# Kernel optimization log

Measured on AMD Instinct MI355X. Metric: run time of the kernel, lower is better.

The kernel has to match this reference:

```python
import jax, jax.numpy as jnp
import numpy as np

B = 65536
N_WORKER, N_PROJECT, EMB = 1807, 2490, 10
STATE_DIM = 2 * EMB          # 20
HIDDEN = 2 * STATE_DIM       # 40
ACTION_DIM = EMB             # 10


def setup_inputs() -> dict:
    key = jax.random.key(0)
    ks = jax.random.split(key, 8)
    worker_ids = jax.random.randint(ks[0], (B,), 0, N_WORKER)
    project_ids = jax.random.randint(ks[1], (B,), 0, N_PROJECT)
    worker_emb = jax.random.normal(ks[2], (N_WORKER, EMB), dtype=jnp.float32)
    project_emb = jax.random.normal(ks[3], (N_PROJECT, EMB), dtype=jnp.float32)
    W1 = jax.random.normal(ks[4], (HIDDEN, STATE_DIM), dtype=jnp.float32) / np.sqrt(STATE_DIM)
    b1 = jnp.zeros((HIDDEN,), dtype=jnp.float32)
    W2 = jax.random.normal(ks[5], (ACTION_DIM, HIDDEN), dtype=jnp.float32) / np.sqrt(HIDDEN)
    b2 = jnp.zeros((ACTION_DIM,), dtype=jnp.float32)
    return {"worker_ids": worker_ids, "project_ids": project_ids,
            "worker_emb": worker_emb, "project_emb": project_emb,
            "W1": W1, "b1": b1, "W2": W2, "b2": b2}


def reference(worker_ids, project_ids, worker_emb, project_emb, W1, b1, W2, b2):
    we = worker_emb[worker_ids]              # [B, 10]
    pe = project_emb[project_ids]            # [B, 10]
    x = jnp.concatenate([we, pe], axis=-1)   # [B, 20]
    h = jax.nn.relu(x @ W1.T + b1)           # [B, 40]
    the_weights = (h @ W2.T + b2)[:, None, :]  # [B, 1, 10]
    # original loop rebuilds rows 1..2489 of the project table -> single slice
    table = project_emb[1:N_PROJECT]         # [2489, 10]
    p = jnp.einsum('bqd,nd->bqn', the_weights, table)  # [B, 1, 2489]
    argmax = jnp.argmax(p, axis=2)           # [B, 1]
    return argmax + 1
```

## Files before the change

kernel.cpp:

```cpp
#include <hip/hip_runtime.h>
#include <float.h>

using v2f = __attribute__((ext_vector_type(2))) float;
using v4f = __attribute__((ext_vector_type(4))) float;

#define EMB 10
#define STATE 20
#define HIDDEN 40
#define NPROJ 2490
#define WAVES 16
#define ITEMS 128

__global__ __launch_bounds__(256, 4) void mlp_kernel(
    const int* __restrict__ wid, const int* __restrict__ pid,
    const float* __restrict__ wemb, const float* __restrict__ pemb,
    const float* __restrict__ W1, const float* __restrict__ b1,
    const float* __restrict__ W2, const float* __restrict__ b2,
    float* __restrict__ ws)
{
    const int b = blockIdx.x * 256 + threadIdx.x;

    const int wi = wid[b];
    const int pi = pid[b];
    const float* __restrict__ wr = wemb + wi * EMB;
    const float* __restrict__ pr = pemb + pi * EMB;
    v2f x2[STATE / 2];
    #pragma unroll
    for (int k = 0; k < EMB / 2; ++k) x2[k] = *(const v2f*)(wr + 2 * k);
    #pragma unroll
    for (int k = 0; k < EMB / 2; ++k) x2[EMB / 2 + k] = *(const v2f*)(pr + 2 * k);

    float hb[HIDDEN];
    #pragma unroll 4
    for (int j = 0; j < HIDDEN; ++j) {
        const v2f* w1r = (const v2f*)(W1 + j * STATE);
        v2f a = w1r[0] * x2[0];
        #pragma unroll
        for (int k = 1; k < STATE / 2; ++k) a += w1r[k] * x2[k];
        hb[j] = fmaxf(a.x + a.y + b1[j], 0.0f);
    }
    v2f h2[HIDDEN / 2];
    #pragma unroll
    for (int k = 0; k < HIDDEN / 2; ++k) h2[k] = (v2f){hb[2 * k], hb[2 * k + 1]};

    v2f* wout = (v2f*)(ws + b * EMB);
    #pragma unroll
    for (int d = 0; d < EMB; d += 2) {
        const v2f* w2r0 = (const v2f*)(W2 + d * HIDDEN);
        const v2f* w2r1 = (const v2f*)(W2 + (d + 1) * HIDDEN);
        v2f a0 = w2r0[0] * h2[0];
        v2f a1 = w2r1[0] * h2[0];
        #pragma unroll
        for (int k = 1; k < HIDDEN / 2; ++k) { a0 += w2r0[k] * h2[k]; a1 += w2r1[k] * h2[k]; }
        wout[d / 2] = (v2f){a0.x + a0.y + b2[d], a1.x + a1.y + b2[d + 1]};
    }
}

__device__ __forceinline__ void score_row(const float* __restrict__ tr, int row,
                                          const float w0[10], const float w1[10],
                                          float best[2], int bidx[2]) {
    float t0 = tr[0], t1 = tr[1], t2 = tr[2], t3 = tr[3], t4 = tr[4];
    float t5 = tr[5], t6 = tr[6], t7 = tr[7], t8 = tr[8], t9 = tr[9];

    float e0 = t0 * w0[0];
    float o0 = t1 * w0[1];
    e0 = fmaf(t2, w0[2], e0);  o0 = fmaf(t3, w0[3], o0);
    e0 = fmaf(t4, w0[4], e0);  o0 = fmaf(t5, w0[5], o0);
    e0 = fmaf(t6, w0[6], e0);  o0 = fmaf(t7, w0[7], o0);
    e0 = fmaf(t8, w0[8], e0);  o0 = fmaf(t9, w0[9], o0);
    float s0 = e0 + o0;

    float e1 = t0 * w1[0];
    float o1 = t1 * w1[1];
    e1 = fmaf(t2, w1[2], e1);  o1 = fmaf(t3, w1[3], o1);
    e1 = fmaf(t4, w1[4], e1);  o1 = fmaf(t5, w1[5], o1);
    e1 = fmaf(t6, w1[6], e1);  o1 = fmaf(t7, w1[7], o1);
    e1 = fmaf(t8, w1[8], e1);  o1 = fmaf(t9, w1[9], o1);
    float s1 = e1 + o1;

    if (s0 > best[0]) { best[0] = s0; bidx[0] = row; }
    if (s1 > best[1]) { best[1] = s1; bidx[1] = row; }
}

template <int P0, int P1>
__device__ __forceinline__ void scan_range(const float* __restrict__ tblf,
                                           const float w0[10], const float w1[10],
                                           float best[2], int bidx[2]) {
    const float* t = tblf + P0 * 20;
    #pragma unroll 4
    for (int p = P0; p < P1; ++p, t += 20) {
        score_row(t,      2 * p,     w0, w1, best, bidx);
        score_row(t + 10, 2 * p + 1, w0, w1, best, bidx);
    }
}

__global__ __launch_bounds__(1024, 8) void scan_kernel(
    const float* __restrict__ pemb, const float* __restrict__ ws,
    int* __restrict__ out)
{
    __shared__ float sb[WAVES][ITEMS];
    __shared__ int   si[WAVES][ITEMS];

    const int tid  = threadIdx.x;
    const int lane = tid & 63;
    const int wave = tid >> 6;
    const int itemBase = blockIdx.x * ITEMS;

    const float* __restrict__ tblf = pemb;

    float w0[10], w1[10];
    {
        const v4f* s0 = (const v4f*)(ws + (itemBase + lane) * EMB);
        const v2f* s0t = (const v2f*)(ws + (itemBase + lane) * EMB + 8);
        v4f a = s0[0], b = s0[1]; v2f c = s0t[0];
        w0[0]=a.x; w0[1]=a.y; w0[2]=a.z; w0[3]=a.w;
        w0[4]=b.x; w0[5]=b.y; w0[6]=b.z; w0[7]=b.w;
        w0[8]=c.x; w0[9]=c.y;
        const v4f* s1 = (const v4f*)(ws + (itemBase + 64 + lane) * EMB);
        const v2f* s1t = (const v2f*)(ws + (itemBase + 64 + lane) * EMB + 8);
        v4f d = s1[0], e = s1[1]; v2f f = s1t[0];
        w1[0]=d.x; w1[1]=d.y; w1[2]=d.z; w1[3]=d.w;
        w1[4]=e.x; w1[5]=e.y; w1[6]=e.z; w1[7]=e.w;
        w1[8]=f.x; w1[9]=f.y;
    }

    float best[2];
    int   bidx[2];
    #pragma unroll
    for (int g = 0; g < 2; ++g) { best[g] = -FLT_MAX; bidx[g] = 1; }

    if (wave == 0) {
        score_row(pemb + 10, 1, w0, w1, best, bidx);
    }

    switch (wave) {
        case  0: scan_range<   1,   79>(tblf, w0, w1, best, bidx); break;
        case  1: scan_range<  79,  157>(tblf, w0, w1, best, bidx); break;
        case  2: scan_range< 157,  235>(tblf, w0, w1, best, bidx); break;
        case  3: scan_range< 235,  313>(tblf, w0, w1, best, bidx); break;
        case  4: scan_range< 313,  391>(tblf, w0, w1, best, bidx); break;
        case  5: scan_range< 391,  469>(tblf, w0, w1, best, bidx); break;
        case  6: scan_range< 469,  547>(tblf, w0, w1, best, bidx); break;
        case  7: scan_range< 547,  625>(tblf, w0, w1, best, bidx); break;
        case  8: scan_range< 625,  703>(tblf, w0, w1, best, bidx); break;
        case  9: scan_range< 703,  781>(tblf, w0, w1, best, bidx); break;
        case 10: scan_range< 781,  859>(tblf, w0, w1, best, bidx); break;
        case 11: scan_range< 859,  937>(tblf, w0, w1, best, bidx); break;
        case 12: scan_range< 937, 1014>(tblf, w0, w1, best, bidx); break;
        case 13: scan_range<1014, 1091>(tblf, w0, w1, best, bidx); break;
        case 14: scan_range<1091, 1168>(tblf, w0, w1, best, bidx); break;
        case 15: scan_range<1168, 1245>(tblf, w0, w1, best, bidx); break;
    }

    sb[wave][lane]      = best[0];
    si[wave][lane]      = bidx[0];
    sb[wave][64 + lane] = best[1];
    si[wave][64 + lane] = bidx[1];
    __syncthreads();

    if (tid < ITEMS) {
        float bb = sb[0][tid];
        int   bi = si[0][tid];
        #pragma unroll
        for (int w = 1; w < WAVES; ++w) {
            float v  = sb[w][tid];
            int   vi = si[w][tid];
            if (v > bb) { bb = v; bi = vi; }
        }
        out[itemBase + tid] = bi;
    }
}

__device__ __forceinline__ void score_pair2(const v4f* __restrict__ tp, int p,
                                            const v2f wv[2][5],
                                            float best[2], int bidx[2]) {
    v4f a0 = tp[0], a1 = tp[1], a2 = tp[2], a3 = tp[3], a4 = tp[4];
    #pragma unroll
    for (int g = 0; g < 2; ++g) {
        v2f c0 = wv[g][0] * a0.lo;
        c0 += wv[g][1] * a0.hi; c0 += wv[g][2] * a1.lo;
        c0 += wv[g][3] * a1.hi; c0 += wv[g][4] * a2.lo;
        float s0 = c0.x + c0.y;
        v2f c1 = wv[g][0] * a2.hi;
        c1 += wv[g][1] * a3.lo; c1 += wv[g][2] * a3.hi;
        c1 += wv[g][3] * a4.lo; c1 += wv[g][4] * a4.hi;
        float s1 = c1.x + c1.y;
        float sp = s0; int ip = 2 * p;
        if (s1 > sp) { sp = s1; ip = 2 * p + 1; }
        if (sp > best[g]) { best[g] = sp; bidx[g] = ip; }
    }
}

__global__ __launch_bounds__(1024, 8) void actor_kernel(
    const int* __restrict__ wid, const int* __restrict__ pid,
    const float* __restrict__ wemb, const float* __restrict__ pemb,
    const float* __restrict__ W1, const float* __restrict__ b1,
    const float* __restrict__ W2, const float* __restrict__ b2,
    int* __restrict__ out)
{
    __shared__ v2f   sw[ITEMS][5];
    __shared__ float sb[WAVES][ITEMS];
    __shared__ int   si[WAVES][ITEMS];

    const int tid  = threadIdx.x;
    const int lane = tid & 63;
    const int wave = tid >> 6;
    const int itemBase = blockIdx.x * ITEMS;

    const v4f* __restrict__ tbl4 =
        (const v4f*)__builtin_assume_aligned(pemb, 16);

    if (wave < ITEMS / 64) {
        const int b = itemBase + wave * 64 + lane;
        const int wi = wid[b];
        const int pi = pid[b];
        const float* __restrict__ wr = wemb + wi * EMB;
        const float* __restrict__ pr = pemb + pi * EMB;
        v2f x2[STATE / 2];
        #pragma unroll
        for (int k = 0; k < EMB / 2; ++k) x2[k] = *(const v2f*)(wr + 2 * k);
        #pragma unroll
        for (int k = 0; k < EMB / 2; ++k) x2[EMB / 2 + k] = *(const v2f*)(pr + 2 * k);

        float hb[HIDDEN];
        #pragma unroll 4
        for (int j = 0; j < HIDDEN; ++j) {
            const v2f* w1r = (const v2f*)(W1 + j * STATE);
            v2f a = w1r[0] * x2[0];
            #pragma unroll
            for (int k = 1; k < STATE / 2; ++k) a += w1r[k] * x2[k];
            hb[j] = fmaxf(a.x + a.y + b1[j], 0.0f);
        }
        v2f h2[HIDDEN / 2];
        #pragma unroll
        for (int k = 0; k < HIDDEN / 2; ++k) h2[k] = (v2f){hb[2 * k], hb[2 * k + 1]};

        #pragma unroll
        for (int d = 0; d < EMB; d += 2) {
            const v2f* w2r0 = (const v2f*)(W2 + d * HIDDEN);
            const v2f* w2r1 = (const v2f*)(W2 + (d + 1) * HIDDEN);
            v2f a0 = w2r0[0] * h2[0];
            v2f a1 = w2r1[0] * h2[0];
            #pragma unroll
            for (int k = 1; k < HIDDEN / 2; ++k) { a0 += w2r0[k] * h2[k]; a1 += w2r1[k] * h2[k]; }
            sw[wave * 64 + lane][d / 2] = (v2f){a0.x + a0.y + b2[d], a1.x + a1.y + b2[d + 1]};
        }
    }
    __syncthreads();

    v2f wv[2][5];
    #pragma unroll
    for (int g = 0; g < 2; ++g) {
        #pragma unroll
        for (int k = 0; k < 5; ++k) wv[g][k] = sw[g * 64 + lane][k];
    }

    float best[2];
    int   bidx[2];
    #pragma unroll
    for (int g = 0; g < 2; ++g) { best[g] = -FLT_MAX; bidx[g] = 1; }

    if (wave == 0) {
        v2f c0v = *(const v2f*)(pemb + 10);
        v4f c1v = *(const v4f*)(pemb + 12);
        v4f c2v = *(const v4f*)(pemb + 16);
        #pragma unroll
        for (int g = 0; g < 2; ++g) {
            v2f a = wv[g][0] * c0v;
            a += wv[g][1] * c1v.lo; a += wv[g][2] * c1v.hi;
            a += wv[g][3] * c2v.lo; a += wv[g][4] * c2v.hi;
            best[g] = a.x + a.y; bidx[g] = 1;
        }
    }

    int start = (wave < 12) ? (1 + 78 * wave) : (937 + 77 * (wave - 12));
    int cnt   = (wave < 12) ? 78 : 77;
    start = __builtin_amdgcn_readfirstlane(start);
    cnt   = __builtin_amdgcn_readfirstlane(cnt);

    const v4f* tp = tbl4 + start * 5;
    #pragma unroll 4
    for (int i = 0; i < cnt; ++i, tp += 5)
        score_pair2(tp, start + i, wv, best, bidx);

    #pragma unroll
    for (int g = 0; g < 2; ++g) {
        sb[wave][g * 64 + lane] = best[g];
        si[wave][g * 64 + lane] = bidx[g];
    }
    __syncthreads();

    if (tid < ITEMS) {
        float bb = sb[0][tid];
        int   bi = si[0][tid];
        #pragma unroll
        for (int w = 1; w < WAVES; ++w) {
            float v  = sb[w][tid];
            int   vi = si[w][tid];
            if (v > bb) { bb = v; bi = vi; }
        }
        out[itemBase + tid] = bi;
    }
}

extern "C" void kernel_launch(void* const* d_in, const int* in_sizes, int n_in,
                              void* d_out, int out_size, void* d_ws, size_t ws_size,
                              hipStream_t stream) {
    const int*   wid  = (const int*)  d_in[0];
    const int*   pid  = (const int*)  d_in[1];
    const float* wemb = (const float*)d_in[2];
    const float* pemb = (const float*)d_in[3];
    const float* W1   = (const float*)d_in[4];
    const float* b1   = (const float*)d_in[5];
    const float* W2   = (const float*)d_in[6];
    const float* b2   = (const float*)d_in[7];
    int* out = (int*)d_out;

    const int B = in_sizes[0];
    const size_t ws_needed = (size_t)B * EMB * sizeof(float);

    if (d_ws != nullptr && ws_size >= ws_needed) {
        float* ws = (float*)d_ws;
        mlp_kernel<<<B / 256, 256, 0, stream>>>(wid, pid, wemb, pemb, W1, b1, W2, b2, ws);
        scan_kernel<<<B / ITEMS, 1024, 0, stream>>>(pemb, ws, out);
    } else {
        actor_kernel<<<B / ITEMS, 1024, 0, stream>>>(wid, pid, wemb, pemb, W1, b1, W2, b2, out);
    }
}
```

Before: 129.6 us.

## Split table scan across slices with 4 items per thread and combine pass

Replaces the scan kernel with a scan4 kernel. Each thread now holds four items' weight vectors and scores every loaded table row against all four, so each row load is reused four times. The project table is also split into 8 slices across blocks, which gives more parallel blocks. A third combine kernel then reduces the per-slice partial argmax results. This trades one extra launch and workspace traffic for better register reuse of table rows and more parallelism.

```diff
diff --git a/kernel.cpp b/kernel.cpp
--- a/kernel.cpp
+++ b/kernel.cpp
@@ -10,6 +10,8 @@
 #define NPROJ 2490
 #define WAVES 16
 #define ITEMS 128
+#define GITEMS 256
+#define NSLICE 8
 
 __global__ __launch_bounds__(256, 4) void mlp_kernel(
     const int* __restrict__ wid, const int* __restrict__ pid,
@@ -54,6 +56,112 @@
         for (int k = 1; k < HIDDEN / 2; ++k) { a0 += w2r0[k] * h2[k]; a1 += w2r1[k] * h2[k]; }
         wout[d / 2] = (v2f){a0.x + a0.y + b2[d], a1.x + a1.y + b2[d + 1]};
     }
+}
+
+__device__ __forceinline__ void score_row4(const float* __restrict__ tr, int row,
+                                           const float w[4][10],
+                                           float best[4], int bidx[4]) {
+    float t0 = tr[0], t1 = tr[1], t2 = tr[2], t3 = tr[3], t4 = tr[4];
+    float t5 = tr[5], t6 = tr[6], t7 = tr[7], t8 = tr[8], t9 = tr[9];
+    #pragma unroll
+    for (int g = 0; g < 4; ++g) {
+        float e = t0 * w[g][0];
+        float o = t1 * w[g][1];
+        e = fmaf(t2, w[g][2], e);  o = fmaf(t3, w[g][3], o);
+        e = fmaf(t4, w[g][4], e);  o = fmaf(t5, w[g][5], o);
+        e = fmaf(t6, w[g][6], e);  o = fmaf(t7, w[g][7], o);
+        e = fmaf(t8, w[g][8], e);  o = fmaf(t9, w[g][9], o);
+        float s = e + o;
+        if (s > best[g]) { best[g] = s; bidx[g] = row; }
+    }
+}
+
+__global__ __launch_bounds__(256, 6) void scan4_kernel(
+    const float* __restrict__ pemb, const float* __restrict__ wsW,
+    float* __restrict__ wsF, int* __restrict__ wsI)
+{
+    __shared__ float sb[4][GITEMS];
+    __shared__ int   si[4][GITEMS];
+
+    const int tid   = threadIdx.x;
+    const int lane  = tid & 63;
+    const int wave  = tid >> 6;
+    const int group = blockIdx.x >> 3;
+    const int slice = blockIdx.x & 7;
+    const int itemBase = group * GITEMS;
+
+    float w[4][10];
+    #pragma unroll
+    for (int g = 0; g < 4; ++g) {
+        const float* base = wsW + (itemBase + g * 64 + lane) * EMB;
+        v4f a = *(const v4f*)(base);
+        v4f b = *(const v4f*)(base + 4);
+        v2f c = *(const v2f*)(base + 8);
+        w[g][0]=a.x; w[g][1]=a.y; w[g][2]=a.z; w[g][3]=a.w;
+        w[g][4]=b.x; w[g][5]=b.y; w[g][6]=b.z; w[g][7]=b.w;
+        w[g][8]=c.x; w[g][9]=c.y;
+    }
+
+    float best[4];
+    int   bidx[4];
+    #pragma unroll
+    for (int g = 0; g < 4; ++g) { best[g] = -FLT_MAX; bidx[g] = 1; }
+
+    int sstart = (slice < 4) ? (1 + 156 * slice) : (625 + 155 * (slice - 4));
+    int wstart = sstart + wave * 39;
+    int wcnt   = (slice < 4) ? 39 : ((wave < 3) ? 39 : 38);
+    wstart = __builtin_amdgcn_readfirstlane(wstart);
+    wcnt   = __builtin_amdgcn_readfirstlane(wcnt);
+
+    if (slice == 0 && wave == 0) {
+        score_row4(pemb + 10, 1, w, best, bidx);
+    }
+
+    const float* t = pemb + wstart * 20;
+    #pragma unroll 2
+    for (int i = 0; i < wcnt; ++i, t += 20) {
+        score_row4(t,      2 * (wstart + i),     w, best, bidx);
+        score_row4(t + 10, 2 * (wstart + i) + 1, w, best, bidx);
+    }
+
+    #pragma unroll
+    for (int g = 0; g < 4; ++g) {
+        sb[wave][g * 64 + lane] = best[g];
+        si[wave][g * 64 + lane] = bidx[g];
+    }
+    __syncthreads();
+
+    {
+        float bb = sb[0][tid];
+        int   bi = si[0][tid];
+        #pragma unroll
+        for (int wv = 1; wv < 4; ++wv) {
+            float v  = sb[wv][tid];
+            int   vi = si[wv][tid];
+            if (v > bb) { bb = v; bi = vi; }
+        }
+        wsF[blockIdx.x * GITEMS + tid] = bb;
+        wsI[blockIdx.x * GITEMS + tid] = bi;
+    }
+}
+
+__global__ __launch_bounds__(256, 8) void combine_kernel(
+    const float* __restrict__ wsF, const int* __restrict__ wsI,
+    int* __restrict__ out)
+{
+    const int i = blockIdx.x * 256 + threadIdx.x;
+    const int g = i >> 8;
+    const int l = i & 255;
+    const int base = g * NSLICE * GITEMS + l;
+    float bb = wsF[base];
+    int   bi = wsI[base];
+    #pragma unroll
+    for (int s = 1; s < NSLICE; ++s) {
+        float v  = wsF[base + s * GITEMS];
+        int   vi = wsI[base + s * GITEMS];
+        if (v > bb) { bb = v; bi = vi; }
+    }
+    out[i] = bi;
 }
 
 __device__ __forceinline__ void score_row(const float* __restrict__ tr, int row,
@@ -317,9 +425,21 @@
     int* out = (int*)d_out;
 
     const int B = in_sizes[0];
-    const size_t ws_needed = (size_t)B * EMB * sizeof(float);
-
-    if (d_ws != nullptr && ws_size >= ws_needed) {
+    const int nGroups = B / GITEMS;
+    const int nBlocks = nGroups * NSLICE;
+
+    const size_t wsW_bytes = (size_t)B * EMB * sizeof(float);
+    const size_t wsF_bytes = (size_t)nBlocks * GITEMS * sizeof(float);
+    const size_t wsI_bytes = (size_t)nBlocks * GITEMS * sizeof(int);
+
+    if (d_ws != nullptr && ws_size >= wsW_bytes + wsF_bytes + wsI_bytes) {
+        float* wsW = (float*)d_ws;
+        float* wsF = (float*)((char*)d_ws + wsW_bytes);
+        int*   wsI = (int*)  ((char*)d_ws + wsW_bytes + wsF_bytes);
+        mlp_kernel<<<B / 256, 256, 0, stream>>>(wid, pid, wemb, pemb, W1, b1, W2, b2, wsW);
+        scan4_kernel<<<nBlocks, 256, 0, stream>>>(pemb, wsW, wsF, wsI);
+        combine_kernel<<<B / 256, 256, 0, stream>>>(wsF, wsI, out);
+    } else if (d_ws != nullptr && ws_size >= wsW_bytes) {
         float* ws = (float*)d_ws;
         mlp_kernel<<<B / 256, 256, 0, stream>>>(wid, pid, wemb, pemb, W1, b1, W2, b2, ws);
         scan_kernel<<<B / ITEMS, 1024, 0, stream>>>(pemb, ws, out);
```

Result: no change. 128.3 us (-1.0%).
